# Optimization experiments

Measured on AMD Instinct MI355X. Metric: run time of the kernel, lower is better.

## Reference

```python
import jax, jax.numpy as jnp
import numpy as np

N_NODES = 100000


def _sage_conv(x, src, dst, w_self, w_neigh, b):
    # DGL SAGEConv('mean'): fc_self(x) + fc_neigh(mean of in-neighbor feats) + bias
    msgs = x[src]                                        # [E, d] gather
    agg = jax.ops.segment_sum(msgs, dst, num_segments=N_NODES)   # [N, d]
    deg = jax.ops.segment_sum(jnp.ones_like(dst, dtype=x.dtype), dst,
                              num_segments=N_NODES)      # [N]
    mean = agg / jnp.maximum(deg, 1.0)[:, None]          # zero-degree -> 0
    return x @ w_self + mean @ w_neigh + b


def setup_inputs() -> dict:
    key = jax.random.key(0)
    ks = jax.random.split(key, 8)
    E, D_IN, D_HID, D_OUT = 1000000, 64, 64, 32
    features = jax.random.normal(ks[0], (N_NODES, D_IN), dtype=jnp.float32)
    src = jax.random.randint(ks[1], (E,), 0, N_NODES, dtype=jnp.int32)
    dst = jax.random.randint(ks[2], (E,), 0, N_NODES, dtype=jnp.int32)
    s = lambda k, i, o: jax.random.normal(k, (i, o), dtype=jnp.float32) / np.sqrt(i)
    return {
        "features": features, "src": src, "dst": dst,
        "w_self1": s(ks[3], D_IN, D_HID), "w_neigh1": s(ks[4], D_IN, D_HID),
        "b1": jnp.zeros((D_HID,), jnp.float32),
        "w_self2": s(ks[5], D_HID, D_OUT), "w_neigh2": s(ks[6], D_HID, D_OUT),
        "b2": jnp.zeros((D_OUT,), jnp.float32),
    }


def reference(features, src, dst, w_self1, w_neigh1, b1, w_self2, w_neigh2, b2):
    h = _sage_conv(features, src, dst, w_self1, w_neigh1, b1)
    h = jax.nn.relu(h)
    # dropout: identity (inference mode)
    h = _sage_conv(h, src, dst, w_self2, w_neigh2, b2)
    return h
```

## Files before the change

kernel.cpp:

```cpp
#include <hip/hip_runtime.h>


#define SPAN        128
#define SPAN_SHIFT  7
#define PART_BLOCK  1024
#define PART_EPT    4
#define NBMAX       1024
#define LDS_S       72

typedef __attribute__((ext_vector_type(8))) short bf16x8;
typedef __attribute__((ext_vector_type(4))) float f32x4;

__device__ __forceinline__ unsigned bf16_rne(float f) {
    unsigned u = __float_as_uint(f);
    return (u + 0x7FFFu + ((u >> 16) & 1u)) >> 16;
}
__device__ __forceinline__ float bf_lo(unsigned u) { return __uint_as_float(u << 16); }
__device__ __forceinline__ float bf_hi(unsigned u) { return __uint_as_float(u & 0xFFFF0000u); }

__global__ __launch_bounds__(PART_BLOCK) void k_partition(
    const int* __restrict__ src, const int* __restrict__ dst,
    int* __restrict__ cursor, unsigned int* __restrict__ pairs,
    int E, int cap,
    const float* __restrict__ feat, unsigned short* __restrict__ xh, long total8,
    const float* __restrict__ ws1, const float* __restrict__ wn1,
    const float* __restrict__ ws2, const float* __restrict__ wn2,
    unsigned short* __restrict__ wt)
{
    const int tid = threadIdx.x;
    for (long i = (long)blockIdx.x * PART_BLOCK + tid; i < total8;
         i += (long)gridDim.x * PART_BLOCK) {
        const float4 a = ((const float4*)feat)[i * 2];
        const float4 b = ((const float4*)feat)[i * 2 + 1];
        uint4 o;
        o.x = bf16_rne(a.x) | (bf16_rne(a.y) << 16);
        o.y = bf16_rne(a.z) | (bf16_rne(a.w) << 16);
        o.z = bf16_rne(b.x) | (bf16_rne(b.y) << 16);
        o.w = bf16_rne(b.z) | (bf16_rne(b.w) << 16);
        ((uint4*)xh)[i] = o;
    }
    if (blockIdx.x < 12) {
        int j = blockIdx.x * PART_BLOCK + tid;
        int mat = j >> 12, rem = j & 4095;
        int c = rem >> 6, k = rem & 63;
        float v;
        if (mat == 0)      v = ws1[k * 64 + c];
        else if (mat == 1) v = wn1[k * 64 + c];
        else               v = (c < 32) ? wn2[k * 32 + c] : ws2[k * 32 + (c - 32)];
        wt[(mat << 12) + (c << 6) + k] = (unsigned short)bf16_rne(v);
    }

    __shared__ int cnt[NBMAX];
    __shared__ int gbase[NBMAX];
    __shared__ int lcur[NBMAX];
    cnt[tid] = 0; lcur[tid] = 0;
    __syncthreads();

    int sv[PART_EPT], bv[PART_EPT];
    const int e0 = blockIdx.x * (PART_BLOCK * PART_EPT) + tid;
    #pragma unroll
    for (int j = 0; j < PART_EPT; ++j) {
        int e = e0 + j * PART_BLOCK;
        bv[j] = -1;
        if (e < E) {
            int s = src[e], d = dst[e];
            bv[j] = d >> SPAN_SHIFT;
            sv[j] = s | ((d & (SPAN - 1)) << 24);
            atomicAdd(&cnt[bv[j]], 1);
        }
    }
    __syncthreads();
    if (cnt[tid] > 0) gbase[tid] = atomicAdd(&cursor[tid], cnt[tid]);
    __syncthreads();
    #pragma unroll
    for (int j = 0; j < PART_EPT; ++j) {
        if (bv[j] >= 0) {
            int r = gbase[bv[j]] + atomicAdd(&lcur[bv[j]], 1);
            if (r < cap) pairs[(size_t)bv[j] * cap + r] = (unsigned int)sv[j];
        }
    }
}

__global__ __launch_bounds__(256) void k_bucket_csr(
    unsigned int* __restrict__ pairs,
    const int* __restrict__ cursor,
    int* __restrict__ starts, int* __restrict__ degs,
    int N, int cap)
{
    __shared__ int cnt[SPAN];
    __shared__ int pref[SPAN];
    __shared__ int lcur[SPAN];
    extern __shared__ unsigned int sorted[];
    const int tid = threadIdx.x;
    const int b = blockIdx.x;
    if (tid < SPAN) { cnt[tid] = 0; lcur[tid] = 0; }
    __syncthreads();

    int m = cursor[b]; if (m > cap) m = cap;
    const size_t pb = (size_t)b * cap;

    for (int i = tid; i < m; i += 256)
        atomicAdd(&cnt[pairs[pb + i] >> 24], 1);
    __syncthreads();

    if (tid < SPAN) pref[tid] = cnt[tid];
    __syncthreads();
    for (int off = 1; off < SPAN; off <<= 1) {
        int v = 0;
        if (tid < SPAN && tid >= off) v = pref[tid - off];
        __syncthreads();
        if (tid < SPAN) pref[tid] += v;
        __syncthreads();
    }

    for (int i = tid; i < m; i += 256) {
        unsigned int p = pairs[pb + i];
        int r = p >> 24;
        int base = (r == 0) ? 0 : pref[r - 1];
        int pos = base + atomicAdd(&lcur[r], 1);
        sorted[pos] = p & 0xFFFFFFu;
    }
    __syncthreads();
    for (int i = tid; i < m; i += 256) pairs[pb + i] = sorted[i];
    if (tid < SPAN) {
        int node = (b << SPAN_SHIFT) + tid;
        if (node < N) {
            int base = (tid == 0) ? 0 : pref[tid - 1];
            starts[node] = (int)pb + base;
            degs[node]   = cnt[tid];
        }
    }
}

__global__ __launch_bounds__(256) void k_gather_fused(
    const unsigned short* __restrict__ xh,
    const unsigned int* __restrict__ esrc,
    const int* __restrict__ starts, const int* __restrict__ degs,
    const unsigned short* __restrict__ wt,
    const float* __restrict__ b1, const float* __restrict__ b2,
    unsigned short* __restrict__ t2,
    float* __restrict__ outp,
    int n)
{
    __shared__ __align__(16) unsigned short sM[16 * LDS_S];
    __shared__ __align__(16) unsigned short sH[16 * LDS_S];
    const int w = threadIdx.x >> 6, lane = threadIdx.x & 63;
    const int quad = lane >> 4, lm = lane & 15;
    const int gm0  = blockIdx.x * 16;
    const int v0   = gm0 + w * 4;

    int e[4], end[4], dg[4];
    #pragma unroll
    for (int j = 0; j < 4; ++j) {
        int v = v0 + j;
        if (v < n) { int b = starts[v]; dg[j] = degs[v]; e[j] = b + quad; end[j] = b + dg[j]; }
        else { dg[j] = 0; e[j] = 0; end[j] = 0; }
    }
    float ga[4][4];
    #pragma unroll
    for (int j = 0; j < 4; ++j)
        #pragma unroll
        for (int k = 0; k < 4; ++k) ga[j][k] = 0.f;

    while ((e[0] < end[0]) | (e[1] < end[1]) | (e[2] < end[2]) | (e[3] < end[3])) {
        uint2 u[4]; float m[4];
        #pragma unroll
        for (int j = 0; j < 4; ++j) {
            bool p = e[j] < end[j];
            m[j] = p ? 1.f : 0.f;
            int idx = p ? e[j] : 0;
            int s = (int)(esrc[idx] & 0xFFFFFFu);
            s = s < n ? s : n - 1;
            u[j] = *(const uint2*)&xh[(size_t)s * 64 + lm * 4];
        }
        #pragma unroll
        for (int j = 0; j < 4; ++j) {
            ga[j][0] = fmaf(m[j], bf_lo(u[j].x), ga[j][0]);
            ga[j][1] = fmaf(m[j], bf_hi(u[j].x), ga[j][1]);
            ga[j][2] = fmaf(m[j], bf_lo(u[j].y), ga[j][2]);
            ga[j][3] = fmaf(m[j], bf_hi(u[j].y), ga[j][3]);
            e[j] += 4;
        }
    }
    #pragma unroll
    for (int j = 0; j < 4; ++j) {
        #pragma unroll
        for (int d = 16; d <= 32; d <<= 1) {
            #pragma unroll
            for (int k = 0; k < 4; ++k) ga[j][k] += __shfl_xor(ga[j][k], d);
        }
        if (lane < 16) {
            float f = dg[j] ? 1.f / (float)dg[j] : 0.f;
            uint2 o;
            o.x = bf16_rne(ga[j][0] * f) | (bf16_rne(ga[j][1] * f) << 16);
            o.y = bf16_rne(ga[j][2] * f) | (bf16_rne(ga[j][3] * f) << 16);
            *(uint2*)&sM[(w * 4 + j) * LDS_S + lm * 4] = o;
        }
    }
    __syncthreads();

    f32x4 acc1 = (f32x4){0.f, 0.f, 0.f, 0.f};
    const int rowG = gm0 + lm;
    const int rA = rowG < n ? rowG : n - 1;
    #pragma unroll
    for (int kt = 0; kt < 2; ++kt) {
        bf16x8 a  = *(const bf16x8*)&xh[(size_t)rA * 64 + kt * 32 + quad * 8];
        bf16x8 am = *(const bf16x8*)&sM[lm * LDS_S + kt * 32 + quad * 8];
        bf16x8 bs = *(const bf16x8*)&wt[((w * 16 + lm) << 6) + kt * 32 + quad * 8];
        bf16x8 bn = *(const bf16x8*)&wt[(1 << 12) + ((w * 16 + lm) << 6) + kt * 32 + quad * 8];
        acc1 = __builtin_amdgcn_mfma_f32_16x16x32_bf16(a,  bs, acc1, 0, 0, 0);
        acc1 = __builtin_amdgcn_mfma_f32_16x16x32_bf16(am, bn, acc1, 0, 0, 0);
    }
    {
        float bb = b1[w * 16 + lm];
        #pragma unroll
        for (int r = 0; r < 4; ++r) {
            float hv = fmaxf(acc1[r] + bb, 0.f);
            sH[(quad * 4 + r) * LDS_S + w * 16 + lm] = (unsigned short)bf16_rne(hv);
        }
    }
    __syncthreads();

    f32x4 acc2 = (f32x4){0.f, 0.f, 0.f, 0.f};
    #pragma unroll
    for (int kt = 0; kt < 2; ++kt) {
        bf16x8 a = *(const bf16x8*)&sH[lm * LDS_S + kt * 32 + quad * 8];
        bf16x8 b = *(const bf16x8*)&wt[(2 << 12) + ((w * 16 + lm) << 6) + kt * 32 + quad * 8];
        acc2 = __builtin_amdgcn_mfma_f32_16x16x32_bf16(a, b, acc2, 0, 0, 0);
    }
    if (w < 2) {
        #pragma unroll
        for (int r = 0; r < 4; ++r) {
            int gm = gm0 + quad * 4 + r;
            if (gm < n)
                t2[(size_t)gm * 32 + w * 16 + lm] = (unsigned short)bf16_rne(acc2[r]);
        }
    } else {
        float bb = b2[(w - 2) * 16 + lm];
        #pragma unroll
        for (int r = 0; r < 4; ++r) {
            int gm = gm0 + quad * 4 + r;
            if (gm < n)
                outp[(size_t)gm * 32 + (w - 2) * 16 + lm] = acc2[r] + bb;
        }
    }
}

__global__ __launch_bounds__(256) void k_gather_b32add(
    const unsigned short* __restrict__ t2,
    const unsigned int* __restrict__ esrc,
    const int* __restrict__ starts, const int* __restrict__ degs,
    float* __restrict__ outp, int n)
{
    const int w = threadIdx.x >> 6, lane = threadIdx.x & 63;
    const int g = lane >> 3, c = lane & 7;
    const int v0 = (blockIdx.x * 4 + w) * 4;
    if (v0 >= n) return;

    int e[4], end[4], deg[4];
    #pragma unroll
    for (int j = 0; j < 4; ++j) {
        int v = v0 + j;
        if (v < n) { int b = starts[v]; deg[j] = degs[v]; e[j] = b + g; end[j] = b + deg[j]; }
        else { deg[j] = 0; e[j] = 0; end[j] = 0; }
    }
    float acc[4][4];
    #pragma unroll
    for (int j = 0; j < 4; ++j)
        #pragma unroll
        for (int k = 0; k < 4; ++k) acc[j][k] = 0.f;

    while ((e[0] < end[0]) | (e[1] < end[1]) | (e[2] < end[2]) | (e[3] < end[3])) {
        uint2 u[4]; float m[4];
        #pragma unroll
        for (int j = 0; j < 4; ++j) {
            bool p = e[j] < end[j];
            m[j] = p ? 1.f : 0.f;
            int idx = p ? e[j] : 0;
            int s = (int)(esrc[idx] & 0xFFFFFFu);
            s = s < n ? s : n - 1;
            u[j] = *(const uint2*)&t2[(size_t)s * 32 + c * 4];
        }
        #pragma unroll
        for (int j = 0; j < 4; ++j) {
            acc[j][0] = fmaf(m[j], bf_lo(u[j].x), acc[j][0]);
            acc[j][1] = fmaf(m[j], bf_hi(u[j].x), acc[j][1]);
            acc[j][2] = fmaf(m[j], bf_lo(u[j].y), acc[j][2]);
            acc[j][3] = fmaf(m[j], bf_hi(u[j].y), acc[j][3]);
            e[j] += 8;
        }
    }
    #pragma unroll
    for (int j = 0; j < 4; ++j) {
        #pragma unroll
        for (int d = 8; d <= 32; d <<= 1) {
            #pragma unroll
            for (int k = 0; k < 4; ++k) acc[j][k] += __shfl_xor(acc[j][k], d);
        }
        if (lane < 8 && v0 + j < n && deg[j] > 0) {
            float f = 1.f / (float)deg[j];
            float4 o = *(const float4*)&outp[(size_t)(v0 + j) * 32 + c * 4];
            o.x += acc[j][0] * f; o.y += acc[j][1] * f;
            o.z += acc[j][2] * f; o.w += acc[j][3] * f;
            *(float4*)&outp[(size_t)(v0 + j) * 32 + c * 4] = o;
        }
    }
}

extern "C" void kernel_launch(void* const* d_in, const int* in_sizes, int n_in,
                              void* d_out, int out_size, void* d_ws, size_t ws_size,
                              hipStream_t stream) {
    const float* feat = (const float*)d_in[0];
    const int*   src  = (const int*)d_in[1];
    const int*   dst  = (const int*)d_in[2];
    const float* ws1  = (const float*)d_in[3];
    const float* wn1  = (const float*)d_in[4];
    const float* b1   = (const float*)d_in[5];
    const float* ws2  = (const float*)d_in[6];
    const float* wn2  = (const float*)d_in[7];
    const float* b2   = (const float*)d_in[8];
    float* out = (float*)d_out;

    const int N = in_sizes[0] / 64;
    const int E = in_sizes[1];
    const int nB = (N + SPAN - 1) >> SPAN_SHIFT;

    int cap = ((E + nB - 1) / nB);
    cap = ((cap + cap / 4) + 63) & ~63;
    {
        size_t fixedBytes = NBMAX * 4 + 3 * 4096 * 2 + (size_t)N * 8
                          + (size_t)N * 64 * 2
                          + (size_t)N * 32 * 2
                          + 16384;
        size_t remain = (ws_size > fixedBytes) ? (ws_size - fixedBytes) : 0;
        size_t capMax = remain / ((size_t)nB * 4);
        if ((size_t)cap > capMax) cap = (int)(capMax & ~(size_t)3);
    }

    char* base = (char*)d_ws;
    int* cursor = (int*)base;
    unsigned short* wt = (unsigned short*)(base + NBMAX * 4);
    unsigned int* pairs = (unsigned int*)(base + NBMAX * 4 + 24576);
    size_t sOff = ((size_t)NBMAX * 4 + 24576 + (size_t)nB * cap * 4 + 4096 + 255) & ~(size_t)255;
    int* starts = (int*)(base + sOff);
    int* degs   = starts + N;
    size_t mOff = (sOff + (size_t)N * 8 + 255) & ~(size_t)255;
    unsigned short* xh = (unsigned short*)(base + mOff);
    unsigned short* t2 = xh + (size_t)N * 64;

    hipMemsetAsync(cursor, 0, NBMAX * 4, stream);

    const long total8 = (long)N * 64 / 8;
    const int pblocks = (E + PART_BLOCK * PART_EPT - 1) / (PART_BLOCK * PART_EPT);
    k_partition<<<pblocks, PART_BLOCK, 0, stream>>>(
        src, dst, cursor, pairs, E, cap,
        feat, xh, total8, ws1, wn1, ws2, wn2, wt);
    k_bucket_csr<<<nB, 256, (size_t)cap * 4, stream>>>(pairs, cursor, starts, degs, N, cap);

    const int gblocks = (N + 15) / 16;

    k_gather_fused<<<gblocks, 256, 0, stream>>>(
        xh, pairs, starts, degs, wt, b1, b2, t2, out, N);
    k_gather_b32add<<<gblocks, 256, 0, stream>>>(t2, pairs, starts, degs, out, N);
}
```

Before: 184.0 us.

## Widen fused gather to 16-byte loads and 32 nodes per block

The fused layer-1 gather kernel now has each lane load 8 bf16 values (16 bytes) per edge instead of 4. Each wave processes 8 nodes, two per 32-lane half, so a block covers 32 nodes and the MFMA stages run two M tiles per wave. The intent is fewer, wider memory transactions in the gather, plus reuse of the weight fragments across two row tiles with half as many blocks. In exchange the kernel uses more registers (8 accumulators per node slot), which may lower occupancy, and each half-wave of 8-lane groups has to hide latency with fewer lanes in flight per node.

Measured after the change: 185.4 us. No clear change (+0.8%).

```diff
diff --git a/kernel.cpp b/kernel.cpp
--- a/kernel.cpp
+++ b/kernel.cpp
@@ -142,28 +142,31 @@
     float* __restrict__ outp,
     int n)
 {
-    __shared__ __align__(16) unsigned short sM[16 * LDS_S];
-    __shared__ __align__(16) unsigned short sH[16 * LDS_S];
+    __shared__ __align__(16) unsigned short sM[32 * LDS_S];
+    __shared__ __align__(16) unsigned short sH[32 * LDS_S];
     const int w = threadIdx.x >> 6, lane = threadIdx.x & 63;
     const int quad = lane >> 4, lm = lane & 15;
-    const int gm0  = blockIdx.x * 16;
-    const int v0   = gm0 + w * 4;
+    const int half = lane >> 5;
+    const int q    = (lane >> 3) & 3;
+    const int c    = lane & 7;
+    const int gm0  = blockIdx.x * 32;
+    const int v0   = gm0 + w * 8;
 
     int e[4], end[4], dg[4];
     #pragma unroll
     for (int j = 0; j < 4; ++j) {
-        int v = v0 + j;
-        if (v < n) { int b = starts[v]; dg[j] = degs[v]; e[j] = b + quad; end[j] = b + dg[j]; }
+        int v = v0 + j * 2 + half;
+        if (v < n) { int b = starts[v]; dg[j] = degs[v]; e[j] = b + q; end[j] = b + dg[j]; }
         else { dg[j] = 0; e[j] = 0; end[j] = 0; }
     }
-    float ga[4][4];
+    float ga[4][8];
     #pragma unroll
     for (int j = 0; j < 4; ++j)
         #pragma unroll
-        for (int k = 0; k < 4; ++k) ga[j][k] = 0.f;
+        for (int k = 0; k < 8; ++k) ga[j][k] = 0.f;
 
     while ((e[0] < end[0]) | (e[1] < end[1]) | (e[2] < end[2]) | (e[3] < end[3])) {
-        uint2 u[4]; float m[4];
+        uint4 u[4]; float m[4];
         #pragma unroll
         for (int j = 0; j < 4; ++j) {
             bool p = e[j] < end[j];
@@ -171,7 +174,7 @@
             int idx = p ? e[j] : 0;
             int s = (int)(esrc[idx] & 0xFFFFFFu);
             s = s < n ? s : n - 1;
-            u[j] = *(const uint2*)&xh[(size_t)s * 64 + lm * 4];
+            u[j] = *(const uint4*)&xh[(size_t)s * 64 + c * 8];
         }
         #pragma unroll
         for (int j = 0; j < 4; ++j) {
@@ -179,69 +182,93 @@
             ga[j][1] = fmaf(m[j], bf_hi(u[j].x), ga[j][1]);
             ga[j][2] = fmaf(m[j], bf_lo(u[j].y), ga[j][2]);
             ga[j][3] = fmaf(m[j], bf_hi(u[j].y), ga[j][3]);
+            ga[j][4] = fmaf(m[j], bf_lo(u[j].z), ga[j][4]);
+            ga[j][5] = fmaf(m[j], bf_hi(u[j].z), ga[j][5]);
+            ga[j][6] = fmaf(m[j], bf_lo(u[j].w), ga[j][6]);
+            ga[j][7] = fmaf(m[j], bf_hi(u[j].w), ga[j][7]);
             e[j] += 4;
         }
     }
     #pragma unroll
     for (int j = 0; j < 4; ++j) {
         #pragma unroll
-        for (int d = 16; d <= 32; d <<= 1) {
-            #pragma unroll
-            for (int k = 0; k < 4; ++k) ga[j][k] += __shfl_xor(ga[j][k], d);
-        }
-        if (lane < 16) {
+        for (int d = 8; d <= 16; d <<= 1) {
+            #pragma unroll
+            for (int k = 0; k < 8; ++k) ga[j][k] += __shfl_xor(ga[j][k], d);
+        }
+        int v = v0 + j * 2 + half;
+        if ((lane & 24) == 0 && v < n) {
             float f = dg[j] ? 1.f / (float)dg[j] : 0.f;
-            uint2 o;
+            uint4 o;
             o.x = bf16_rne(ga[j][0] * f) | (bf16_rne(ga[j][1] * f) << 16);
             o.y = bf16_rne(ga[j][2] * f) | (bf16_rne(ga[j][3] * f) << 16);
-            *(uint2*)&sM[(w * 4 + j) * LDS_S + lm * 4] = o;
-        }
-    }
-    __syncthreads();
-
-    f32x4 acc1 = (f32x4){0.f, 0.f, 0.f, 0.f};
-    const int rowG = gm0 + lm;
-    const int rA = rowG < n ? rowG : n - 1;
-    #pragma unroll
-    for (int kt = 0; kt < 2; ++kt) {
-        bf16x8 a  = *(const bf16x8*)&xh[(size_t)rA * 64 + kt * 32 + quad * 8];
-        bf16x8 am = *(const bf16x8*)&sM[lm * LDS_S + kt * 32 + quad * 8];
-        bf16x8 bs = *(const bf16x8*)&wt[((w * 16 + lm) << 6) + kt * 32 + quad * 8];
-        bf16x8 bn = *(const bf16x8*)&wt[(1 << 12) + ((w * 16 + lm) << 6) + kt * 32 + quad * 8];
-        acc1 = __builtin_amdgcn_mfma_f32_16x16x32_bf16(a,  bs, acc1, 0, 0, 0);
-        acc1 = __builtin_amdgcn_mfma_f32_16x16x32_bf16(am, bn, acc1, 0, 0, 0);
+            o.z = bf16_rne(ga[j][4] * f) | (bf16_rne(ga[j][5] * f) << 16);
+            o.w = bf16_rne(ga[j][6] * f) | (bf16_rne(ga[j][7] * f) << 16);
+            *(uint4*)&sM[(w * 8 + j * 2 + half) * LDS_S + c * 8] = o;
+        }
+    }
+    __syncthreads();
+
+    f32x4 acc1[2];
+    acc1[0] = (f32x4){0.f, 0.f, 0.f, 0.f};
+    acc1[1] = (f32x4){0.f, 0.f, 0.f, 0.f};
+    #pragma unroll
+    for (int mt = 0; mt < 2; ++mt) {
+        const int rowG = gm0 + mt * 16 + lm;
+        const int rA = rowG < n ? rowG : n - 1;
+        #pragma unroll
+        for (int kt = 0; kt < 2; ++kt) {
+            bf16x8 a  = *(const bf16x8*)&xh[(size_t)rA * 64 + kt * 32 + quad * 8];
+            bf16x8 am = *(const bf16x8*)&sM[(mt * 16 + lm) * LDS_S + kt * 32 + quad * 8];
+            bf16x8 bs = *(const bf16x8*)&wt[((w * 16 + lm) << 6) + kt * 32 + quad * 8];
+            bf16x8 bn = *(const bf16x8*)&wt[(1 << 12) + ((w * 16 + lm) << 6) + kt * 32 + quad * 8];
+            acc1[mt] = __builtin_amdgcn_mfma_f32_16x16x32_bf16(a,  bs, acc1[mt], 0, 0, 0);
+            acc1[mt] = __builtin_amdgcn_mfma_f32_16x16x32_bf16(am, bn, acc1[mt], 0, 0, 0);
+        }
     }
     {
         float bb = b1[w * 16 + lm];
         #pragma unroll
-        for (int r = 0; r < 4; ++r) {
-            float hv = fmaxf(acc1[r] + bb, 0.f);
-            sH[(quad * 4 + r) * LDS_S + w * 16 + lm] = (unsigned short)bf16_rne(hv);
-        }
-    }
-    __syncthreads();
-
-    f32x4 acc2 = (f32x4){0.f, 0.f, 0.f, 0.f};
-    #pragma unroll
-    for (int kt = 0; kt < 2; ++kt) {
-        bf16x8 a = *(const bf16x8*)&sH[lm * LDS_S + kt * 32 + quad * 8];
-        bf16x8 b = *(const bf16x8*)&wt[(2 << 12) + ((w * 16 + lm) << 6) + kt * 32 + quad * 8];
-        acc2 = __builtin_amdgcn_mfma_f32_16x16x32_bf16(a, b, acc2, 0, 0, 0);
-    }
-    if (w < 2) {
-        #pragma unroll
-        for (int r = 0; r < 4; ++r) {
-            int gm = gm0 + quad * 4 + r;
-            if (gm < n)
-                t2[(size_t)gm * 32 + w * 16 + lm] = (unsigned short)bf16_rne(acc2[r]);
-        }
-    } else {
-        float bb = b2[(w - 2) * 16 + lm];
-        #pragma unroll
-        for (int r = 0; r < 4; ++r) {
-            int gm = gm0 + quad * 4 + r;
-            if (gm < n)
-                outp[(size_t)gm * 32 + (w - 2) * 16 + lm] = acc2[r] + bb;
+        for (int mt = 0; mt < 2; ++mt) {
+            #pragma unroll
+            for (int r = 0; r < 4; ++r) {
+                float hv = fmaxf(acc1[mt][r] + bb, 0.f);
+                sH[(mt * 16 + quad * 4 + r) * LDS_S + w * 16 + lm] =
+                    (unsigned short)bf16_rne(hv);
+            }
+        }
+    }
+    __syncthreads();
+
+    f32x4 acc2[2];
+    acc2[0] = (f32x4){0.f, 0.f, 0.f, 0.f};
+    acc2[1] = (f32x4){0.f, 0.f, 0.f, 0.f};
+    #pragma unroll
+    for (int mt = 0; mt < 2; ++mt) {
+        #pragma unroll
+        for (int kt = 0; kt < 2; ++kt) {
+            bf16x8 a = *(const bf16x8*)&sH[(mt * 16 + lm) * LDS_S + kt * 32 + quad * 8];
+            bf16x8 b = *(const bf16x8*)&wt[(2 << 12) + ((w * 16 + lm) << 6) + kt * 32 + quad * 8];
+            acc2[mt] = __builtin_amdgcn_mfma_f32_16x16x32_bf16(a, b, acc2[mt], 0, 0, 0);
+        }
+    }
+    #pragma unroll
+    for (int mt = 0; mt < 2; ++mt) {
+        if (w < 2) {
+            #pragma unroll
+            for (int r = 0; r < 4; ++r) {
+                int gm = gm0 + mt * 16 + quad * 4 + r;
+                if (gm < n)
+                    t2[(size_t)gm * 32 + w * 16 + lm] = (unsigned short)bf16_rne(acc2[mt][r]);
+            }
+        } else {
+            float bb = b2[(w - 2) * 16 + lm];
+            #pragma unroll
+            for (int r = 0; r < 4; ++r) {
+                int gm = gm0 + mt * 16 + quad * 4 + r;
+                if (gm < n)
+                    outp[(size_t)gm * 32 + (w - 2) * 16 + lm] = acc2[mt][r] + bb;
+            }
         }
     }
 }
@@ -357,9 +384,10 @@
         feat, xh, total8, ws1, wn1, ws2, wn2, wt);
     k_bucket_csr<<<nB, 256, (size_t)cap * 4, stream>>>(pairs, cursor, starts, degs, N, cap);
 
+    const int fblocks = (N + 31) / 32;
     const int gblocks = (N + 15) / 16;
 
-    k_gather_fused<<<gblocks, 256, 0, stream>>>(
+    k_gather_fused<<<fblocks, 256, 0, stream>>>(
         xh, pairs, starts, degs, wt, b1, b2, t2, out, N);
     k_gather_b32add<<<gblocks, 256, 0, stream>>>(t2, pairs, starts, degs, out, N);
 }
```
